# Kernel tuning notes

Hardware: AMD Instinct MI355X
Metric: run time of the kernel (lower is better)

Reference implementation:

```python
import jax, jax.numpy as jnp
from jax import lax
import numpy as np

B, T = 512, 20
RES, C3D, AUD, P, H, NC = 2048, 4096, 128, 1024, 1024, 200


def setup_inputs() -> dict:
    key = jax.random.key(0)
    ks = jax.random.split(key, 40)

    def n(k, shape, s=0.02):
        return jax.random.normal(k, shape, jnp.float32) * s

    inp = {
        "resnet_features": jax.random.normal(ks[0], (B, T, RES), jnp.float32),
        "c3d_features": jax.random.normal(ks[1], (B, T, C3D), jnp.float32),
        "audio_features": jax.random.normal(ks[2], (B, T, AUD), jnp.float32),
        "W_audio": n(ks[3], (P, AUD)), "b_audio": jnp.zeros((P,), jnp.float32),
        "W_resnet": n(ks[4], (P, RES)), "b_resnet": jnp.zeros((P,), jnp.float32),
        "W_c3d": n(ks[5], (P, C3D)), "b_c3d": jnp.zeros((P,), jnp.float32),
    }
    i = 6
    for nm in ["audio_fwd", "audio_rev", "resnet_fwd", "resnet_rev", "c3d_fwd", "c3d_rev"]:
        inp[nm + "_Wih"] = n(ks[i], (4 * H, P)); i += 1
        inp[nm + "_Whh"] = n(ks[i], (4 * H, H)); i += 1
        inp[nm + "_bih"] = jnp.zeros((4 * H,), jnp.float32)
        inp[nm + "_bhh"] = jnp.zeros((4 * H,), jnp.float32)
    inp["W_out"] = n(ks[i], (NC, 2 * H)); i += 1
    inp["b_out"] = jnp.zeros((NC,), jnp.float32)
    return inp


def _run_lstm(xs, Wih, Whh, bih, bhh, reverse):
    # xs: (B, T, P). PyTorch LSTMCell gate order: i, f, g, o.
    b = bih + bhh

    def step(carry, x):
        h, c = carry
        gates = x @ Wih.T + h @ Whh.T + b  # (B, 4H)
        i, f, g, o = jnp.split(gates, 4, axis=-1)
        c = jax.nn.sigmoid(f) * c + jax.nn.sigmoid(i) * jnp.tanh(g)
        h = jax.nn.sigmoid(o) * jnp.tanh(c)
        return (h, c), None

    bsz = xs.shape[0]
    init = (jnp.zeros((bsz, H), xs.dtype), jnp.zeros((bsz, H), xs.dtype))
    (h, c), _ = lax.scan(step, init, jnp.swapaxes(xs, 0, 1), reverse=reverse)
    return h


def reference(resnet_features, c3d_features, audio_features, W_audio, b_audio, W_resnet, b_resnet, W_c3d, b_c3d, audio_fwd_Wih, audio_fwd_Whh, audio_fwd_bih, audio_fwd_bhh, audio_rev_Wih, audio_rev_Whh, audio_rev_bih, audio_rev_bhh, resnet_fwd_Wih, resnet_fwd_Whh, resnet_fwd_bih, resnet_fwd_bhh, resnet_rev_Wih, resnet_rev_Whh, resnet_rev_bih, resnet_rev_bhh, c3d_fwd_Wih, c3d_fwd_Whh, c3d_fwd_bih, c3d_fwd_bhh, c3d_rev_Wih, c3d_rev_Whh, c3d_rev_bih, c3d_rev_bhh, W_out, b_out):
    # Dropouts are identity in eval mode.
    out_a = audio_features @ W_audio.T + b_audio    # (B, T, P)
    out_r = resnet_features @ W_resnet.T + b_resnet
    out_c = c3d_features @ W_c3d.T + b_c3d

    h_af = _run_lstm(out_a, audio_fwd_Wih, audio_fwd_Whh, audio_fwd_bih, audio_fwd_bhh, False)
    h_ar = _run_lstm(out_a, audio_rev_Wih, audio_rev_Whh, audio_rev_bih, audio_rev_bhh, True)
    h_rf = _run_lstm(out_r, resnet_fwd_Wih, resnet_fwd_Whh, resnet_fwd_bih, resnet_fwd_bhh, False)
    h_rr = _run_lstm(out_r, resnet_rev_Wih, resnet_rev_Whh, resnet_rev_bih, resnet_rev_bhh, True)
    h_cf = _run_lstm(out_c, c3d_fwd_Wih, c3d_fwd_Whh, c3d_fwd_bih, c3d_fwd_bhh, False)
    h_cr = _run_lstm(out_c, c3d_rev_Wih, c3d_rev_Whh, c3d_rev_bih, c3d_rev_bhh, True)

    audio_final = jnp.concatenate([h_af, h_ar], axis=1)
    resnet_final = jnp.concatenate([h_rf, h_rr], axis=1)
    c3d_final = jnp.concatenate([h_cf, h_cr], axis=1)
    fused = audio_final * resnet_final * c3d_final  # (B, 2H)
    return fused @ W_out.T + b_out  # (B, NC)
```

## Files before the change

### kernel.cpp

```cpp
#include <hip/hip_runtime.h>
#include <cstdio>
#include <cstdint>

#define TT    20
#define BATCH 512
#define HID   1024
#define G4    4096
#define NG    8192
#define BT    (BATCH * TT)
#define NCLS  200
#define SH    ((size_t)BATCH * HID)

typedef unsigned short u16;
typedef __attribute__((ext_vector_type(8))) short short8;
typedef __attribute__((ext_vector_type(4))) float f32x4;
typedef __attribute__((ext_vector_type(4))) unsigned short u16x4;

__device__ __forceinline__ float sigf(float x) { return 1.0f / (1.0f + __expf(-x)); }

__device__ __forceinline__ u16 f2bf(float x) {
    unsigned u = __float_as_uint(x);
    u += 0x7FFFu + ((u >> 16) & 1u);
    return (u16)(u >> 16);
}
__device__ __forceinline__ float bf2f(u16 b) { return __uint_as_float(((unsigned)b) << 16); }

__device__ __forceinline__ void gld16(const u16* g, u16* l) {
    __builtin_amdgcn_global_load_lds(
        (const __attribute__((address_space(1))) void*)g,
        (__attribute__((address_space(3))) void*)l, 16, 0, 0);
}

__global__ void cvt4_kernel(const float* __restrict__ x, u16* __restrict__ y, int n4)
{
    const int stride = gridDim.x * blockDim.x;
    for (int i = blockIdx.x * blockDim.x + threadIdx.x; i < n4; i += stride) {
        const float4 v = ((const float4*)x)[i];
        uint2 hp;
        hp.x = (unsigned)f2bf(v.x) | ((unsigned)f2bf(v.y) << 16);
        hp.y = (unsigned)f2bf(v.z) | ((unsigned)f2bf(v.w) << 16);
        ((uint2*)y)[i] = hp;
    }
}

struct CvtJob { const float* src; u16* dst; };
struct CvtBatch { CvtJob j[6]; };
__global__ void cvt4_batch(CvtBatch cb, int n4)
{
    const float* __restrict__ x = cb.j[blockIdx.y].src;
    u16* __restrict__ y = cb.j[blockIdx.y].dst;
    const int stride = gridDim.x * blockDim.x;
    for (int i = blockIdx.x * blockDim.x + threadIdx.x; i < n4; i += stride) {
        const float4 v = ((const float4*)x)[i];
        uint2 hp;
        hp.x = (unsigned)f2bf(v.x) | ((unsigned)f2bf(v.y) << 16);
        hp.y = (unsigned)f2bf(v.z) | ((unsigned)f2bf(v.w) << 16);
        ((uint2*)y)[i] = hp;
    }
}

__global__ void bias_cat_kernel(const float* __restrict__ bi0, const float* __restrict__ bh0,
                                const float* __restrict__ bi1, const float* __restrict__ bh1,
                                float* __restrict__ bcat)
{
    const int n = blockIdx.x * blockDim.x + threadIdx.x;
    if (n >= NG) return;
    bcat[n] = (n < G4) ? (bi0[n] + bh0[n]) : (bi1[n - G4] + bh1[n - G4]);
}

template<int MODE>
__launch_bounds__(256)
__global__ void gemm_b16(const u16* __restrict__ A, const u16* __restrict__ W,
                         const float* __restrict__ b1, u16* __restrict__ Cb,
                         int M, int N, int K, int cm)
{
    __shared__ u16 sA[4][128][8]; __shared__ u16 sW[4][128][8];
    const int tid = threadIdx.x, lane = tid & 63, w = tid >> 6;
    const int wr = w >> 1, wc = w & 1;

    const int nwg = gridDim.x;
    const int cpx = nwg >> 3;
    const int lg = (blockIdx.x & 7) * cpx + (blockIdx.x >> 3);
    const int nby = N >> 7;
    const int cb = cm * nby;
    const int chunk = lg / cb;
    const int r = lg - chunk * cb;
    const int m0 = (chunk * cm + (r % cm)) * 128;
    const int n0 = (r / cm) * 128;

    const u16* A0 = A + (size_t)m0 * K;
    const u16* W0 = W + (size_t)n0 * K;

    f32x4 acc[4][4];
#pragma unroll
    for (int i = 0; i < 4; ++i)
#pragma unroll
        for (int j = 0; j < 4; ++j) acc[i][j] = f32x4{0.f, 0.f, 0.f, 0.f};

    const int u1 = tid, u2 = tid + 256;
    const size_t go1 = (size_t)(u1 & 127) * K + (u1 >> 7) * 8;
    const size_t go2 = (size_t)(u2 & 127) * K + (u2 >> 7) * 8;
    u16* const l1 = (u16*)sA + (size_t)u1 * 8;
    u16* const l2 = (u16*)sA + (size_t)u2 * 8;
    const size_t dW = (u16*)sW - (u16*)sA;

    for (int k0 = 0; k0 < K; k0 += 32) {
        gld16(A0 + go1 + k0, l1);       gld16(A0 + go2 + k0, l2);
        gld16(W0 + go1 + k0, l1 + dW);  gld16(W0 + go2 + k0, l2 + dW);
        __syncthreads();

        const int kb = lane >> 4, rr = lane & 15;
        short8 Av[4], Wv[4];
#pragma unroll
        for (int i = 0; i < 4; ++i) {
            Av[i] = *(const short8*)&sA[kb][wr * 64 + i * 16 + rr][0];
            Wv[i] = *(const short8*)&sW[kb][wc * 64 + i * 16 + rr][0];
        }
#pragma unroll
        for (int i = 0; i < 4; ++i)
#pragma unroll
            for (int j = 0; j < 4; ++j)
                acc[i][j] = __builtin_amdgcn_mfma_f32_16x16x32_bf16(Av[i], Wv[j], acc[i][j], 0, 0, 0);
        __syncthreads();
    }

    const int rr = lane & 15, rg = lane >> 4;
#pragma unroll
    for (int j = 0; j < 4; ++j) {
        const int col = n0 + wc * 64 + j * 16 + rr;
        const float bias = b1 ? b1[col] : 0.f;
#pragma unroll
        for (int i = 0; i < 4; ++i) {
            if (MODE == 1) {
                u16x4 pk;
#pragma unroll
                for (int q = 0; q < 4; ++q) pk[q] = f2bf(acc[i][j][q] + bias);
                const int grp = (m0 >> 2) + wr * 16 + i * 4 + rg;
                __builtin_nontemporal_store(pk, (u16x4*)(Cb + ((size_t)grp * N + col) * 4));
            } else {
#pragma unroll
                for (int q = 0; q < 4; ++q) {
                    const int row = m0 + wr * 64 + i * 16 + rg * 4 + q;
                    const int rowp = (row % 20) * 512 + row / 20;
                    Cb[(size_t)rowp * N + col] = f2bf(acc[i][j][q] + bias);
                }
            }
        }
    }
}

__launch_bounds__(256)
__global__ void lstm_step6(const u16* __restrict__ whhAll,
                           const u16* __restrict__ Gall,
                           const u16* __restrict__ hinAll,
                           u16* __restrict__ houtAll,
                           float* __restrict__ cbAll,
                           float* __restrict__ hfinAll,
                           int s, int write_hfin)
{
    const int l = blockIdx.z;
    __shared__ u16 sA[2][4][64][8];
    __shared__ u16 sW[2][4][128][8];
    const int tid = threadIdx.x, lane = tid & 63, w = tid >> 6;
    const int wr = w >> 1, wc = w & 1;
    const int j0 = blockIdx.x * 32;
    const int m0 = blockIdx.y * 64;

    const u16* __restrict__ hin = hinAll + (size_t)l * SH;
    const u16* __restrict__ Whh = whhAll + (size_t)l * G4 * HID;
    const int do_gemm = (s > 0);

    f32x4 acc[2][4];
#pragma unroll
    for (int i = 0; i < 2; ++i)
#pragma unroll
        for (int g = 0; g < 4; ++g) acc[i][g] = f32x4{0.f, 0.f, 0.f, 0.f};

    const int rr = lane & 15, rg = lane >> 4;

    if (do_gemm) {
        const size_t goA = (size_t)(m0 + (tid & 63)) * HID + (tid >> 6) * 8;
        const int rW = tid & 127;
        const int wrow = ((rW >> 4) & 3) * HID + j0 + (rW >> 6) * 16 + (rW & 15);
        const size_t goW1 = (size_t)wrow * HID + (tid >> 7) * 8;
        const size_t goW2 = (size_t)wrow * HID + ((tid >> 7) + 2) * 8;
        u16* const ldA  = (u16*)sA + (size_t)tid * 8;
        u16* const ldW1 = (u16*)sW + (size_t)tid * 8;
        u16* const ldW2 = (u16*)sW + (size_t)(tid + 256) * 8;

        gld16(hin + goA,  ldA);
        gld16(Whh + goW1, ldW1);
        gld16(Whh + goW2, ldW2);
        __syncthreads();

        for (int k0 = 0; k0 < HID; k0 += 32) {
            const int bf = (k0 >> 5) & 1;
            if (k0 + 32 < HID) {
                gld16(hin + goA  + k0 + 32, ldA  + (bf ^ 1) * 2048);
                gld16(Whh + goW1 + k0 + 32, ldW1 + (bf ^ 1) * 4096);
                gld16(Whh + goW2 + k0 + 32, ldW2 + (bf ^ 1) * 4096);
            }
            const int kb = lane >> 4;
            short8 Av[2], Wv[4];
#pragma unroll
            for (int i = 0; i < 2; ++i)
                Av[i] = *(const short8*)&sA[bf][kb][wr * 32 + i * 16 + rr][0];
#pragma unroll
            for (int g = 0; g < 4; ++g)
                Wv[g] = *(const short8*)&sW[bf][kb][wc * 64 + g * 16 + rr][0];
#pragma unroll
            for (int i = 0; i < 2; ++i)
#pragma unroll
                for (int g = 0; g < 4; ++g)
                    acc[i][g] = __builtin_amdgcn_mfma_f32_16x16x32_bf16(Av[i], Wv[g], acc[i][g], 0, 0, 0);
            __syncthreads();
        }
    }

    const int j = j0 + wc * 16 + rr;
    const int t = (l & 1) ? (TT - 1 - s) : s;
    const u16* __restrict__ Gl = Gall + (size_t)(l >> 1) * BT * NG;
    const int cbase = (l & 1) * G4 + j;
    float* __restrict__ cb = cbAll + (size_t)l * SH;
    float* __restrict__ hf = hfinAll + (size_t)l * SH;
    u16* __restrict__ ho = houtAll + (size_t)l * SH;
#pragma unroll
    for (int i = 0; i < 2; ++i) {
        const int grp = t * 128 + (m0 >> 2) + wr * 8 + i * 4 + rg;
        const u16* gb = Gl + (size_t)grp * NG * 4;
        const u16x4 g0 = __builtin_nontemporal_load((const u16x4*)(gb + (size_t)cbase * 4));
        const u16x4 g1 = __builtin_nontemporal_load((const u16x4*)(gb + (size_t)(cbase + 1024) * 4));
        const u16x4 g2 = __builtin_nontemporal_load((const u16x4*)(gb + (size_t)(cbase + 2048) * 4));
        const u16x4 g3 = __builtin_nontemporal_load((const u16x4*)(gb + (size_t)(cbase + 3072) * 4));
#pragma unroll
        for (int q = 0; q < 4; ++q) {
            const int b = m0 + wr * 32 + i * 16 + rg * 4 + q;
            const float pi = acc[i][0][q] + bf2f(g0[q]);
            const float pf = acc[i][1][q] + bf2f(g1[q]);
            const float pg = acc[i][2][q] + bf2f(g2[q]);
            const float po = acc[i][3][q] + bf2f(g3[q]);
            const size_t idx = (size_t)b * HID + j;
            const float cprev = do_gemm ? cb[idx] : 0.f;
            const float cn = sigf(pf) * cprev + sigf(pi) * tanhf(pg);
            cb[idx] = cn;
            const float h = sigf(po) * tanhf(cn);
            if (write_hfin) hf[idx] = h;
            else            ho[idx] = f2bf(h);
        }
    }
}

__global__ void fuse_mul_kernel(const float* __restrict__ hfin, float* __restrict__ fused)
{
    const int idx = blockIdx.x * blockDim.x + threadIdx.x;
    if (idx >= BATCH * 2 * HID) return;
    const int b = idx >> 11;
    const int n = idx & 2047;
    const int half = n >> 10;
    const int j = n & 1023;
    const size_t o = (size_t)b * HID + j;
    fused[idx] = hfin[(size_t)(0 + half) * SH + o] *
                 hfin[(size_t)(2 + half) * SH + o] *
                 hfin[(size_t)(4 + half) * SH + o];
}

__launch_bounds__(256)
__global__ void gemm_bias_kernel(const float* __restrict__ A, const float* __restrict__ W,
                                 const float* __restrict__ b1,
                                 float* __restrict__ C, int M, int N, int K)
{
    __shared__ float As[16][68];
    __shared__ float Ws[16][68];
    const int tid = threadIdx.x;
    const int tx = tid & 15, ty = tid >> 4;
    const int m0 = blockIdx.x * 64;
    const int n0 = blockIdx.y * 64;
    const int lr = tid >> 2;
    const int lk = (tid & 3) << 2;
    const bool mok = (m0 + lr < M);
    const bool nok = (n0 + lr < N);
    const float* Arow = A + (size_t)(m0 + lr) * K + lk;
    const float* Wrow = W + (size_t)(n0 + lr) * K + lk;
    float acc[4][4] = {};

    for (int k0 = 0; k0 < K; k0 += 16) {
        float4 av = make_float4(0.f, 0.f, 0.f, 0.f);
        float4 wv = make_float4(0.f, 0.f, 0.f, 0.f);
        if (mok) av = *(const float4*)(Arow + k0);
        if (nok) wv = *(const float4*)(Wrow + k0);
        As[lk + 0][lr] = av.x; As[lk + 1][lr] = av.y; As[lk + 2][lr] = av.z; As[lk + 3][lr] = av.w;
        Ws[lk + 0][lr] = wv.x; Ws[lk + 1][lr] = wv.y; Ws[lk + 2][lr] = wv.z; Ws[lk + 3][lr] = wv.w;
        __syncthreads();
#pragma unroll
        for (int k = 0; k < 16; ++k) {
            const float4 a = *(const float4*)&As[k][ty << 2];
            const float4 ww = *(const float4*)&Ws[k][tx << 2];
            const float a4[4] = {a.x, a.y, a.z, a.w};
            const float w4[4] = {ww.x, ww.y, ww.z, ww.w};
#pragma unroll
            for (int i = 0; i < 4; ++i)
#pragma unroll
                for (int j = 0; j < 4; ++j)
                    acc[i][j] = fmaf(a4[i], w4[j], acc[i][j]);
        }
        __syncthreads();
    }

#pragma unroll
    for (int i = 0; i < 4; ++i) {
        const int m = m0 + (ty << 2) + i;
        if (m >= M) continue;
#pragma unroll
        for (int j = 0; j < 4; ++j) {
            const int n = n0 + (tx << 2) + j;
            if (n >= N) continue;
            C[(size_t)m * N + n] = acc[i][j] + (b1 ? b1[n] : 0.f);
        }
    }
}

extern "C" void kernel_launch(void* const* d_in, const int* in_sizes, int n_in,
                              void* d_out, int out_size, void* d_ws, size_t ws_size,
                              hipStream_t stream)
{
    const float* resnet   = (const float*)d_in[0];
    const float* c3d      = (const float*)d_in[1];
    const float* audio    = (const float*)d_in[2];
    const float* W_audio  = (const float*)d_in[3];
    const float* b_audio  = (const float*)d_in[4];
    const float* W_resnet = (const float*)d_in[5];
    const float* b_resnet = (const float*)d_in[6];
    const float* W_c3d    = (const float*)d_in[7];
    const float* b_c3d    = (const float*)d_in[8];
    const float* Wih[6]; const float* Whh[6]; const float* bih[6]; const float* bhh[6];
    for (int l = 0; l < 6; ++l) {
        Wih[l] = (const float*)d_in[9 + 4 * l];
        Whh[l] = (const float*)d_in[10 + 4 * l];
        bih[l] = (const float*)d_in[11 + 4 * l];
        bhh[l] = (const float*)d_in[12 + 4 * l];
    }
    const float* W_out = (const float*)d_in[33];
    const float* b_out = (const float*)d_in[34];
    float* out = (float*)d_out;

    const float* feat[3] = { audio, resnet, c3d };
    const float* fw[3]   = { W_audio, W_resnet, W_c3d };
    const float* fb[3]   = { b_audio, b_resnet, b_c3d };
    const int    fK[3]   = { 128, 2048, 4096 };

    char* p = (char*)d_ws;
    char* pend = p + ws_size;
    auto alloc = [&](size_t bytes) -> void* {
        void* q = p; p += (bytes + 255) & ~(size_t)255; return q;
    };
    const size_t FW = (size_t)1024 * (128 + 2048 + 4096);
    u16* Gall  = (u16*)alloc((size_t)3 * BT * NG * 2);
    u16* featB = Gall + (size_t)2 * BT * NG;
    u16* fwB   = (u16*)alloc(FW * 2);
    u16* wihB  = (u16*)alloc((size_t)NG * HID * 2);
    u16* whhB  = (u16*)alloc((size_t)3 * NG * HID * 2);
    u16* projB = (u16*)alloc((size_t)BT * HID * 2);
    float* bcat = (float*)alloc((size_t)NG * 4);
    u16* hA    = (u16*)alloc((size_t)6 * SH * 2);
    u16* hB    = (u16*)alloc((size_t)6 * SH * 2);
    float* cb    = (float*)alloc((size_t)6 * SH * 4);
    float* hfin  = (float*)alloc((size_t)6 * SH * 4);
    float* fused = (float*)alloc((size_t)BATCH * 2 * HID * 4);
    if (p > pend) {
        fprintf(stderr, "kernel_launch: ws too small: need %zu have %zu\n",
                (size_t)(p - (char*)d_ws), ws_size);
        return;
    }

    const dim3 blk(256);
    const size_t fwOff[3] = { 0, (size_t)1024 * 128, (size_t)1024 * 128 + (size_t)1024 * 2048 };
    const int n4w = (G4 * HID) / 4;

    for (int st = 0; st < 3; ++st) {
        const int n4 = (1024 * fK[st]) / 4;
        cvt4_kernel<<<dim3(min(2048, (n4 + 255) / 256)), blk, 0, stream>>>(
            fw[st], fwB + fwOff[st], n4);
    }
    {
        CvtBatch b6;
        for (int l = 0; l < 6; ++l) { b6.j[l].src = Whh[l]; b6.j[l].dst = whhB + (size_t)l * G4 * HID; }
        cvt4_batch<<<dim3(768, 6), blk, 0, stream>>>(b6, n4w);
    }

    for (int st = 0; st < 3; ++st) {
        const int K = fK[st];
        cvt4_kernel<<<dim3(2048), blk, 0, stream>>>(feat[st], featB, (BT * K) / 4);
        gemm_b16<0><<<dim3((BT / 128) * (HID / 128)), blk, 0, stream>>>(
            featB, fwB + fwOff[st], fb[st], projB, BT, HID, K, 8);
        {
            CvtBatch b2;
            for (int d = 0; d < 2; ++d) {
                b2.j[d].src = Wih[st * 2 + d];
                b2.j[d].dst = wihB + (size_t)d * G4 * HID;
            }
            cvt4_batch<<<dim3(768, 2), blk, 0, stream>>>(b2, n4w);
        }
        bias_cat_kernel<<<dim3(NG / 256), blk, 0, stream>>>(
            bih[st * 2], bhh[st * 2], bih[st * 2 + 1], bhh[st * 2 + 1], bcat);
        gemm_b16<1><<<dim3((BT / 128) * (NG / 128)), blk, 0, stream>>>(
            projB, wihB, bcat, Gall + (size_t)st * BT * NG, BT, NG, HID, 8);
    }

    for (int s = 0; s < TT; ++s) {
        const u16* in = (s & 1) ? hB : hA;
        u16*      o  = (s & 1) ? hA : hB;
        lstm_step6<<<dim3(HID / 32, BATCH / 64, 6), blk, 0, stream>>>(
            whhB, Gall, in, o, cb, hfin, s, s == TT - 1 ? 1 : 0);
    }

    fuse_mul_kernel<<<dim3((BATCH * 2 * HID) / 256), blk, 0, stream>>>(hfin, fused);

    gemm_bias_kernel<<<dim3(BATCH / 64, (NCLS + 63) / 64), blk, 0, stream>>>(
        fused, W_out, b_out, out, BATCH, NCLS, 2 * HID);
}
```

Measured before the change: 3.309 ms.

## Fold audio projection into LSTM input weights to shrink audio gate GEMM

For the audio stream the projection (K=128 to P=1024) and the LSTM input GEMM are merged algebraically: Wih·W_audio is precomputed as an 8192x128 combined weight, and the bias vector absorbs Wih·b_audio. The gate GEMM then runs with K=128 straight on the permuted audio features, replacing a K=128 projection GEMM plus a K=1024 gate GEMM. The cost is a small weight-side GEMM and bias reduction each call. Rounding changes slightly because the intermediate projection is no longer quantized to bf16.

```diff
diff --git a/kernel.cpp b/kernel.cpp
--- a/kernel.cpp
+++ b/kernel.cpp
@@ -59,6 +59,53 @@
     }
 }
 
+__global__ void cvtperm_audio(const float* __restrict__ in, u16* __restrict__ out)
+{
+    const int tid4 = blockIdx.x * blockDim.x + threadIdx.x;
+    if (tid4 >= BT * 128 / 4) return;
+    const int row = tid4 >> 5;
+    const int kk  = (tid4 & 31) << 2;
+    const int t = row % 20, b = row / 20;
+    const float4 v = *(const float4*)(in + (size_t)row * 128 + kk);
+    uint2 hp;
+    hp.x = (unsigned)f2bf(v.x) | ((unsigned)f2bf(v.y) << 16);
+    hp.y = (unsigned)f2bf(v.z) | ((unsigned)f2bf(v.w) << 16);
+    *(uint2*)(out + (size_t)(t * 512 + b) * 128 + kk) = hp;
+}
+
+__global__ void transpose_cvt(const float* __restrict__ in, u16* __restrict__ out)
+{
+    const int idx = blockIdx.x * blockDim.x + threadIdx.x;
+    if (idx >= 128 * 1024) return;
+    const int a = idx >> 10, p = idx & 1023;
+    out[idx] = f2bf(in[p * 128 + a]);
+}
+
+__global__ void bvec_kernel(const float* __restrict__ Wih0, const float* __restrict__ Wih1,
+                            const float* __restrict__ ba,
+                            const float* __restrict__ bi0, const float* __restrict__ bh0,
+                            const float* __restrict__ bi1, const float* __restrict__ bh1,
+                            float* __restrict__ bvec)
+{
+    const int wv = blockIdx.x * 4 + (threadIdx.x >> 6);
+    const int lane = threadIdx.x & 63;
+    const float* Wrow = (wv < 4096) ? Wih0 + (size_t)wv * 1024
+                                    : Wih1 + (size_t)(wv - 4096) * 1024;
+    float s = 0.f;
+#pragma unroll
+    for (int c = 0; c < 4; ++c) {
+        const float4 w = *(const float4*)(Wrow + c * 256 + lane * 4);
+        const float4 x = *(const float4*)(ba + c * 256 + lane * 4);
+        s += w.x * x.x + w.y * x.y + w.z * x.z + w.w * x.w;
+    }
+#pragma unroll
+    for (int o = 32; o; o >>= 1) s += __shfl_xor(s, o);
+    if (lane == 0) {
+        const int n = wv & 4095;
+        bvec[wv] = s + ((wv < 4096) ? bi0[n] + bh0[n] : bi1[n] + bh1[n]);
+    }
+}
+
 __global__ void bias_cat_kernel(const float* __restrict__ bi0, const float* __restrict__ bh0,
                                 const float* __restrict__ bi1, const float* __restrict__ bh1,
                                 float* __restrict__ bcat)
@@ -137,12 +184,18 @@
                 for (int q = 0; q < 4; ++q) pk[q] = f2bf(acc[i][j][q] + bias);
                 const int grp = (m0 >> 2) + wr * 16 + i * 4 + rg;
                 __builtin_nontemporal_store(pk, (u16x4*)(Cb + ((size_t)grp * N + col) * 4));
-            } else {
+            } else if (MODE == 0) {
 #pragma unroll
                 for (int q = 0; q < 4; ++q) {
                     const int row = m0 + wr * 64 + i * 16 + rg * 4 + q;
                     const int rowp = (row % 20) * 512 + row / 20;
                     Cb[(size_t)rowp * N + col] = f2bf(acc[i][j][q] + bias);
+                }
+            } else {
+#pragma unroll
+                for (int q = 0; q < 4; ++q) {
+                    const int row = m0 + wr * 64 + i * 16 + rg * 4 + q;
+                    Cb[(size_t)row * N + col] = f2bf(acc[i][j][q] + bias);
                 }
             }
         }
@@ -366,6 +419,10 @@
     float* cb    = (float*)alloc((size_t)6 * SH * 4);
     float* hfin  = (float*)alloc((size_t)6 * SH * 4);
     float* fused = (float*)alloc((size_t)BATCH * 2 * HID * 4);
+    u16* waT      = (u16*)alloc((size_t)128 * 1024 * 2);
+    u16* wcombB   = (u16*)alloc((size_t)NG * 128 * 2);
+    u16* featPerm = (u16*)alloc((size_t)BT * 128 * 2);
+    float* bvec   = (float*)alloc((size_t)NG * 4);
     if (p > pend) {
         fprintf(stderr, "kernel_launch: ws too small: need %zu have %zu\n",
                 (size_t)(p - (char*)d_ws), ws_size);
@@ -376,7 +433,7 @@
     const size_t fwOff[3] = { 0, (size_t)1024 * 128, (size_t)1024 * 128 + (size_t)1024 * 2048 };
     const int n4w = (G4 * HID) / 4;
 
-    for (int st = 0; st < 3; ++st) {
+    for (int st = 1; st < 3; ++st) {
         const int n4 = (1024 * fK[st]) / 4;
         cvt4_kernel<<<dim3(min(2048, (n4 + 255) / 256)), blk, 0, stream>>>(
             fw[st], fwB + fwOff[st], n4);
@@ -387,7 +444,20 @@
         cvt4_batch<<<dim3(768, 6), blk, 0, stream>>>(b6, n4w);
     }
 
-    for (int st = 0; st < 3; ++st) {
+    {
+        CvtBatch b2;
+        for (int d = 0; d < 2; ++d) { b2.j[d].src = Wih[d]; b2.j[d].dst = wihB + (size_t)d * G4 * HID; }
+        cvt4_batch<<<dim3(768, 2), blk, 0, stream>>>(b2, n4w);
+        transpose_cvt<<<dim3(512), blk, 0, stream>>>(W_audio, waT);
+        gemm_b16<2><<<dim3(64), blk, 0, stream>>>(wihB, waT, nullptr, wcombB, NG, 128, 1024, 8);
+        bvec_kernel<<<dim3(2048), blk, 0, stream>>>(
+            Wih[0], Wih[1], b_audio, bih[0], bhh[0], bih[1], bhh[1], bvec);
+        cvtperm_audio<<<dim3((BT * 128 / 4 + 255) / 256), blk, 0, stream>>>(audio, featPerm);
+        gemm_b16<1><<<dim3((BT / 128) * (NG / 128)), blk, 0, stream>>>(
+            featPerm, wcombB, bvec, Gall, BT, NG, 128, 8);
+    }
+
+    for (int st = 1; st < 3; ++st) {
         const int K = fK[st];
         cvt4_kernel<<<dim3(2048), blk, 0, stream>>>(feat[st], featB, (BT * K) / 4);
         gemm_b16<0><<<dim3((BT / 128) * (HID / 128)), blk, 0, stream>>>(
```

Measured after the change: 3.084 ms. 6.8% less time.
